# Kernel optimization log

Measured on AMD Instinct MI355X. Metric: run time of the kernel, lower is better.

The kernel has to match this reference:

```python
import jax, jax.numpy as jnp
import numpy as np

N_NODES = 100000
N_EDGES = 3200000
IN_DIM = 128
HID_DIM = 64
OUT_DIM = 2
N_GRAPHS = 512


def setup_inputs() -> dict:
    key = jax.random.key(0)
    ks = jax.random.split(key, 8)
    x = jax.random.normal(ks[0], (N_NODES, IN_DIM), dtype=jnp.float32)
    edge_index = jax.random.randint(ks[1], (2, N_EDGES), 0, N_NODES, dtype=jnp.int64)
    batch = jnp.sort(jax.random.randint(ks[2], (N_NODES,), 0, N_GRAPHS, dtype=jnp.int64))
    # GCNConv params (glorot-ish scale)
    W_gcn = jax.random.normal(ks[3], (IN_DIM, HID_DIM), dtype=jnp.float32) / np.sqrt(IN_DIM)
    b_gcn = jnp.zeros((HID_DIM,), dtype=jnp.float32)
    # MLP params: Linear(hid,hid) -> ReLU -> Linear(hid,out)
    W1 = jax.random.normal(ks[4], (HID_DIM, HID_DIM), dtype=jnp.float32) / np.sqrt(HID_DIM)
    b1 = jnp.zeros((HID_DIM,), dtype=jnp.float32)
    W2 = jax.random.normal(ks[5], (HID_DIM, OUT_DIM), dtype=jnp.float32) / np.sqrt(HID_DIM)
    b2 = jnp.zeros((OUT_DIM,), dtype=jnp.float32)
    return {"x": x, "edge_index": edge_index, "batch": batch,
            "W_gcn": W_gcn, "b_gcn": b_gcn, "W1": W1, "b1": b1, "W2": W2, "b2": b2}


def reference(x, edge_index, batch, W_gcn, b_gcn, W1, b1, W2, b2):
    n = x.shape[0]
    # --- GCNConv: add self-loops, symmetric normalization, aggregate, transform ---
    self_loop = jnp.arange(n, dtype=edge_index.dtype)
    row = jnp.concatenate([edge_index[0], self_loop])  # source nodes
    col = jnp.concatenate([edge_index[1], self_loop])  # target nodes
    deg = jax.ops.segment_sum(jnp.ones_like(col, dtype=x.dtype), col, num_segments=n)
    dinv = jnp.where(deg > 0, jax.lax.rsqrt(deg), 0.0)
    norm = dinv[row] * dinv[col]                       # (E+N,)
    xw = x @ W_gcn                                     # (N, hid) transform first (in_dim > hid)
    msg = xw[row] * norm[:, None]                      # gather + scale
    z = jax.ops.segment_sum(msg, col, num_segments=n) + b_gcn  # scatter-add
    z = jax.nn.relu(z)
    # --- global mean pool over graphs ---
    sums = jax.ops.segment_sum(z, batch, num_segments=N_GRAPHS)          # (G, hid)
    cnts = jax.ops.segment_sum(jnp.ones((n,), z.dtype), batch, num_segments=N_GRAPHS)
    g = sums / jnp.maximum(cnts, 1.0)[:, None]
    # --- MLP -> sigmoid ---
    h = jax.nn.relu(g @ W1 + b1)
    return jax.nn.sigmoid(h @ W2 + b2)                 # (G, out_dim)
```

## Files before the change

### kernel.cpp

```cpp
#include <hip/hip_runtime.h>

#define N_NODES 100000
#define N_EDGES 3200000
#define IN_DIM 128
#define HID_DIM 64
#define OUT_DIM 2
#define N_GRAPHS 512

#define BSHIFT 6
#define NBUCK 1564
#define NB3 256
#define EPB 12500
#define NSB 391
#define LDS_E2 3072
#define ZERO_ROW N_NODES

__device__ inline int xcol(int b) { return ((b & 7) << 5) | (b >> 3); }

__device__ inline float uaf(unsigned int u) {
    union { unsigned int i; float f; } v; v.i = u; return v.f;
}
__device__ inline unsigned short f2bf(float f) {
    union { float f; unsigned int i; } v; v.f = f;
    unsigned int r = v.i + 0x7fffu + ((v.i >> 16) & 1u);
    return (unsigned short)(r >> 16);
}

typedef __attribute__((ext_vector_type(8))) short bf16x8;
typedef __attribute__((ext_vector_type(4))) float f32x4;
typedef __attribute__((ext_vector_type(2))) float f32x2;

__global__ __launch_bounds__(512) void k_hist(const int* __restrict__ col,
                                              int* __restrict__ H) {
    __shared__ int h[NBUCK];
    for (int i = threadIdx.x; i < NBUCK; i += 512) h[i] = 0;
    __syncthreads();
    int b = blockIdx.x;
    int bb = xcol(b);
    int s = b * EPB, e = s + EPB;
    for (int i = s + threadIdx.x; i < e; i += 512)
        atomicAdd(&h[col[i] >> BSHIFT], 1);
    __syncthreads();
    for (int i = threadIdx.x; i < NBUCK; i += 512)
        H[i * NB3 + bb] = h[i];
}

__global__ __launch_bounds__(1024) void k_scan_a(const int* __restrict__ H,
                                                 int* __restrict__ OFF,
                                                 int* __restrict__ bsum) {
    __shared__ int lds[1024];
    int i = blockIdx.x * 1024 + threadIdx.x;
    int v = H[i];
    lds[threadIdx.x] = v;
    __syncthreads();
    for (int off = 1; off < 1024; off <<= 1) {
        int t = (threadIdx.x >= off) ? lds[threadIdx.x - off] : 0;
        __syncthreads();
        lds[threadIdx.x] += t;
        __syncthreads();
    }
    OFF[i] = lds[threadIdx.x] - v;
    if (threadIdx.x == 1023) bsum[blockIdx.x] = lds[1023];
}

__global__ __launch_bounds__(1024) void k_scan_b(int* __restrict__ OFF,
                                                 const int* __restrict__ bsum,
                                                 float* __restrict__ gsum,
                                                 unsigned char* __restrict__ xws) {
    __shared__ int ls[NSB];
    for (int i = threadIdx.x; i < NSB; i += 1024) ls[i] = bsum[i];
    __syncthreads();
    if (threadIdx.x == 0) {
        int run = 0;
        for (int b = 0; b < NSB; b++) { int t = ls[b]; ls[b] = run; run += t; }
    }
    __syncthreads();
    int i = blockIdx.x * 1024 + threadIdx.x;
    OFF[i] += ls[blockIdx.x];
    if (blockIdx.x < 32) gsum[blockIdx.x * 1024 + threadIdx.x] = 0.f;
    if (blockIdx.x == 32 && threadIdx.x < 16)
        ((int*)(xws + (size_t)ZERO_ROW * HID_DIM))[threadIdx.x] = 0;
}

__global__ __launch_bounds__(512) void k_scatter(const int* __restrict__ row,
                                                 const int* __restrict__ col,
                                                 const int* __restrict__ OFF,
                                                 int* __restrict__ binned) {
    __shared__ int lofs[NBUCK];
    __shared__ int cur[NBUCK];
    int b = blockIdx.x;
    int bb = xcol(b);
    for (int i = threadIdx.x; i < NBUCK; i += 512) {
        lofs[i] = OFF[i * NB3 + bb];
        cur[i] = 0;
    }
    __syncthreads();
    int s = b * EPB, e = s + EPB;
    for (int i = s + threadIdx.x; i < e; i += 512) {
        int c = col[i];
        int r = row[i];
        int bk = c >> BSHIFT;
        int rk = atomicAdd(&cur[bk], 1);
        binned[lofs[bk] + rk] = ((c & 63) << 17) | r;
    }
}

__global__ __launch_bounds__(256) void k_deg(const int* __restrict__ binned,
                                             const int* __restrict__ OFF,
                                             int* __restrict__ degs,
                                             float* __restrict__ dinv) {
    int bkt = blockIdx.x;
    int s = OFF[bkt * NB3];
    int e = (bkt == NBUCK - 1) ? N_EDGES : OFF[(bkt + 1) * NB3];
    __shared__ int cnt[64];
    if (threadIdx.x < 64) cnt[threadIdx.x] = 0;
    __syncthreads();
    for (int i = s + threadIdx.x; i < e; i += 256)
        atomicAdd(&cnt[binned[i] >> 17], 1);
    __syncthreads();
    int n = (bkt << BSHIFT) + threadIdx.x;
    if (threadIdx.x < 64 && n < N_NODES) {
        degs[n] = cnt[threadIdx.x];
        dinv[n] = rsqrtf((float)cnt[threadIdx.x] + 1.0f);
    }
}

__global__ __launch_bounds__(256) void k_gemm(const float* __restrict__ x,
                                              const float* __restrict__ Wg,
                                              const float* __restrict__ dinv,
                                              unsigned char* __restrict__ xws) {
    __shared__ unsigned short wb[16][64][8];

    for (int idx = threadIdx.x; idx < 1024; idx += 256) {
        int f = idx >> 6, l = idx & 63;
        int ks = f >> 2, nt = f & 3;
        int n = (l & 15) + (nt << 4);
        int kbase = (ks << 5) + ((l >> 4) << 3);
        unsigned short tmp[8];
#pragma unroll
        for (int j = 0; j < 8; j++)
            tmp[j] = f2bf(Wg[(kbase + j) * HID_DIM + n]);
        *(bf16x8*)&wb[f][l][0] = *(const bf16x8*)tmp;
    }
    __syncthreads();

    int wave = threadIdx.x >> 6;
    int lane = threadIdx.x & 63;
    int q = lane >> 4, nn = lane & 15;

    bf16x8 bfrag[4][4];
#pragma unroll
    for (int ks = 0; ks < 4; ks++)
#pragma unroll
        for (int nt = 0; nt < 4; nt++)
            bfrag[ks][nt] = *(const bf16x8*)&wb[ks * 4 + nt][lane][0];

    int node0 = blockIdx.x * 64 + wave * 16;
    int arow = node0 + nn;
    if (arow > N_NODES - 1) arow = N_NODES - 1;
    const float* xrow = x + (size_t)arow * IN_DIM + (q << 3);

    f32x4 acc[4] = {{0.f,0.f,0.f,0.f},{0.f,0.f,0.f,0.f},
                    {0.f,0.f,0.f,0.f},{0.f,0.f,0.f,0.f}};
#pragma unroll
    for (int ks = 0; ks < 4; ks++) {
        float4 xa = *(const float4*)(xrow + ks * 32);
        float4 xb_ = *(const float4*)(xrow + ks * 32 + 4);
        bf16x8 af;
        af[0] = (short)f2bf(xa.x); af[1] = (short)f2bf(xa.y);
        af[2] = (short)f2bf(xa.z); af[3] = (short)f2bf(xa.w);
        af[4] = (short)f2bf(xb_.x); af[5] = (short)f2bf(xb_.y);
        af[6] = (short)f2bf(xb_.z); af[7] = (short)f2bf(xb_.w);
#pragma unroll
        for (int nt = 0; nt < 4; nt++)
            acc[nt] = __builtin_amdgcn_mfma_f32_16x16x32_bf16(af, bfrag[ks][nt], acc[nt], 0, 0, 0);
    }

#pragma unroll
    for (int r = 0; r < 4; r++) {
        int mrow = node0 + q * 4 + r;
        if (mrow < N_NODES) {
            float dn = dinv[mrow];
            int p01 = __builtin_amdgcn_cvt_pk_fp8_f32(acc[0][r] * dn, acc[1][r] * dn, 0, false);
            int p23 = __builtin_amdgcn_cvt_pk_fp8_f32(acc[2][r] * dn, acc[3][r] * dn, 0, false);
            unsigned char* rp = xws + (size_t)mrow * HID_DIM + nn;
            rp[0]  = (unsigned char)(p01 & 0xff);
            rp[16] = (unsigned char)((p01 >> 8) & 0xff);
            rp[32] = (unsigned char)(p23 & 0xff);
            rp[48] = (unsigned char)((p23 >> 8) & 0xff);
        }
    }
}

__global__ __launch_bounds__(512) void k_aggrf(const unsigned char* __restrict__ xws,
                                               const int* __restrict__ binned,
                                               const int* __restrict__ OFF,
                                               const int* __restrict__ degs,
                                               const int* __restrict__ batch,
                                               const float* __restrict__ bg,
                                               float* __restrict__ gsum) {
    int bkt = blockIdx.x;
    int nbase = bkt << BSHIFT;
    if (nbase >= N_NODES) return;
    int nnodes = N_NODES - nbase; if (nnodes > 64) nnodes = 64;
    int s = OFF[bkt * NB3];
    int e = (bkt == NBUCK - 1) ? N_EDGES : OFF[(bkt + 1) * NB3];
    int m = e - s;

    __shared__ int cnt[64];
    __shared__ int lptr[65];
    __shared__ int cur[64];
    __shared__ int sb[64];
    __shared__ alignas(16) int srt[LDS_E2];
    __shared__ float pool[8][4][64];

    if (threadIdx.x < 64) {
        int n = nbase + threadIdx.x;
        cnt[threadIdx.x] = (threadIdx.x < nnodes) ? degs[n] : 0;
        sb[threadIdx.x]  = (threadIdx.x < nnodes) ? batch[n] : 0;
        cur[threadIdx.x] = 0;
    }
    for (int t = threadIdx.x; t < 8 * 4 * 64; t += 512)
        ((float*)pool)[t] = 0.f;
    __syncthreads();

    if (threadIdx.x == 0) {
        int run = 0;
        for (int i = 0; i < 64; i++) { lptr[i] = run; run += (cnt[i] + 15) & ~15; }
        lptr[64] = run;
    }
    __syncthreads();
    int tot = lptr[64]; if (tot > LDS_E2) tot = LDS_E2;
    for (int i = threadIdx.x; i < tot; i += 512) srt[i] = ZERO_ROW << 6;
    __syncthreads();
    for (int i = threadIdx.x; i < m; i += 512) {
        int pk = binned[s + i];
        int nid = pk >> 17;
        int rk = atomicAdd(&cur[nid], 1);
        int pos = lptr[nid] + rk;
        if (pos < LDS_E2) srt[pos] = (pk & 0x1FFFF) << 6;
    }
    __syncthreads();

    int wave = threadIdx.x >> 6;
    int lane = threadIdx.x & 63;
    int sub = lane >> 4;
    int lc  = lane & 15;
    int l4  = lc << 2;
    const unsigned char* xb = xws;
    float4 bg4 = ((const float4*)bg)[lc];
    int g0 = sb[0];

    for (int k = 0; k < 8; k++) {
        int ln = wave * 8 + k;
        if (ln >= nnodes) break;
        int n = nbase + ln;
        int s0 = lptr[ln], e0 = lptr[ln + 1];
        unsigned int ds = *(const unsigned int*)(xb + ((size_t)n << 6) + l4);
        f32x4 a0 = {0.f,0.f,0.f,0.f}, a1 = {0.f,0.f,0.f,0.f};
        f32x4 a2 = {0.f,0.f,0.f,0.f}, a3 = {0.f,0.f,0.f,0.f};
        for (int i = s0; i < e0; i += 16) {
            int4 r4 = *(const int4*)&srt[i + (sub << 2)];
            unsigned int d0 = *(const unsigned int*)(xb + r4.x + l4);
            unsigned int d1 = *(const unsigned int*)(xb + r4.y + l4);
            unsigned int d2 = *(const unsigned int*)(xb + r4.z + l4);
            unsigned int d3 = *(const unsigned int*)(xb + r4.w + l4);
            f32x2 p;
            p = __builtin_amdgcn_cvt_pk_f32_fp8(d0, false); a0[0] += p[0]; a0[1] += p[1];
            p = __builtin_amdgcn_cvt_pk_f32_fp8(d0, true);  a0[2] += p[0]; a0[3] += p[1];
            p = __builtin_amdgcn_cvt_pk_f32_fp8(d1, false); a1[0] += p[0]; a1[1] += p[1];
            p = __builtin_amdgcn_cvt_pk_f32_fp8(d1, true);  a1[2] += p[0]; a1[3] += p[1];
            p = __builtin_amdgcn_cvt_pk_f32_fp8(d2, false); a2[0] += p[0]; a2[1] += p[1];
            p = __builtin_amdgcn_cvt_pk_f32_fp8(d2, true);  a2[2] += p[0]; a2[3] += p[1];
            p = __builtin_amdgcn_cvt_pk_f32_fp8(d3, false); a3[0] += p[0]; a3[1] += p[1];
            p = __builtin_amdgcn_cvt_pk_f32_fp8(d3, true);  a3[2] += p[0]; a3[3] += p[1];
        }
        f32x4 t = (a0 + a1) + (a2 + a3);
#pragma unroll
        for (int c = 0; c < 4; c++) {
            float v = t[c];
            v += __shfl_xor(v, 16);
            v += __shfl_xor(v, 32);
            t[c] = v;
        }
        if (sub == 0) {
            f32x2 slo = __builtin_amdgcn_cvt_pk_f32_fp8(ds, false);
            f32x2 shi = __builtin_amdgcn_cvt_pk_f32_fp8(ds, true);
            t[0] += slo[0]; t[1] += slo[1]; t[2] += shi[0]; t[3] += shi[1];
            float dn = rsqrtf((float)cnt[ln] + 1.0f);
            float4 val;
            val.x = fmaxf(t[0] * dn + bg4.x, 0.f);
            val.y = fmaxf(t[1] * dn + bg4.y, 0.f);
            val.z = fmaxf(t[2] * dn + bg4.z, 0.f);
            val.w = fmaxf(t[3] * dn + bg4.w, 0.f);
            int slot = sb[ln] - g0;
            if (slot < 4) {
                float4* pp = (float4*)&pool[wave][slot][l4];
                float4 pv = *pp;
                pv.x += val.x; pv.y += val.y; pv.z += val.z; pv.w += val.w;
                *pp = pv;
            } else {
                atomicAdd(&gsum[sb[ln] * HID_DIM + l4 + 0], val.x);
                atomicAdd(&gsum[sb[ln] * HID_DIM + l4 + 1], val.y);
                atomicAdd(&gsum[sb[ln] * HID_DIM + l4 + 2], val.z);
                atomicAdd(&gsum[sb[ln] * HID_DIM + l4 + 3], val.w);
            }
        }
    }
    __syncthreads();

    for (int t = threadIdx.x; t < 4 * 64; t += 512) {
        int slot = t >> 6, j = t & 63;
        float v = 0.f;
#pragma unroll
        for (int w2 = 0; w2 < 8; w2++) v += pool[w2][slot][j];
        if (v != 0.f) atomicAdd(&gsum[(g0 + slot) * HID_DIM + j], v);
    }
}

__device__ inline int lower_bound_i(const int* __restrict__ a, int n, int v) {
    int lo = 0, hi = n;
    while (lo < hi) {
        int mid = (lo + hi) >> 1;
        if (a[mid] < v) lo = mid + 1; else hi = mid;
    }
    return lo;
}

__global__ __launch_bounds__(64) void k_mlp(const float* __restrict__ gsum,
                                            const int* __restrict__ batch,
                                            const float* __restrict__ W1,
                                            const float* __restrict__ b1,
                                            const float* __restrict__ W2,
                                            const float* __restrict__ b2,
                                            float* __restrict__ out) {
    int g = blockIdx.x;
    int j = threadIdx.x;
    int start = lower_bound_i(batch, N_NODES, g);
    int end   = lower_bound_i(batch, N_NODES, g + 1);
    float cnt = fmaxf((float)(end - start), 1.0f);

    __shared__ float gs[64];
    __shared__ float hs[64];
    gs[j] = gsum[g * 64 + j] / cnt;
    __syncthreads();

    float h = b1[j];
    for (int k = 0; k < 64; k++) h += gs[k] * W1[k * 64 + j];
    hs[j] = fmaxf(h, 0.f);
    __syncthreads();

    if (j < OUT_DIM) {
        float o = b2[j];
        for (int k = 0; k < 64; k++) o += hs[k] * W2[k * OUT_DIM + j];
        out[g * OUT_DIM + j] = 1.f / (1.f + expf(-o));
    }
}

extern "C" void kernel_launch(void* const* d_in, const int* in_sizes, int n_in,
                              void* d_out, int out_size, void* d_ws, size_t ws_size,
                              hipStream_t stream) {
    const float* x   = (const float*)d_in[0];
    const int* eidx  = (const int*)d_in[1];
    const int* batch = (const int*)d_in[2];
    const float* Wg  = (const float*)d_in[3];
    const float* bg  = (const float*)d_in[4];
    const float* W1  = (const float*)d_in[5];
    const float* b1  = (const float*)d_in[6];
    const float* W2  = (const float*)d_in[7];
    const float* b2  = (const float*)d_in[8];
    float* out = (float*)d_out;

    char* w = (char*)d_ws;
    unsigned char* xws = (unsigned char*)w;     w += (size_t)(N_NODES + 1) * HID_DIM;
    int*   binned  = (int*)w;                   w += (size_t)N_EDGES * 4;
    int*   H       = (int*)w;                   w += (size_t)NBUCK * NB3 * 4;
    int*   OFF     = (int*)w;                   w += (size_t)NBUCK * NB3 * 4;
    int*   bsum    = (int*)w;                   w += NSB * 4;
    int*   degs    = (int*)w;                   w += N_NODES * 4;
    float* dinv    = (float*)w;                 w += N_NODES * 4;
    float* gsum    = (float*)w;                 w += N_GRAPHS * HID_DIM * 4;

    const int* rowp = eidx;
    const int* colp = eidx + N_EDGES;

    k_hist<<<NB3, 512, 0, stream>>>(colp, H);
    k_scan_a<<<NSB, 1024, 0, stream>>>(H, OFF, bsum);
    k_scan_b<<<NSB, 1024, 0, stream>>>(OFF, bsum, gsum, xws);
    k_scatter<<<NB3, 512, 0, stream>>>(rowp, colp, OFF, binned);
    k_deg<<<NBUCK, 256, 0, stream>>>(binned, OFF, degs, dinv);
    k_gemm<<<(N_NODES + 63) / 64, 256, 0, stream>>>(x, Wg, dinv, xws);
    k_aggrf<<<NBUCK, 512, 0, stream>>>(xws, binned, OFF, degs, batch, bg, gsum);
    k_mlp<<<N_GRAPHS, 64, 0, stream>>>(gsum, batch, W1, b1, W2, b2, out);
}
```

Baseline: 213.3 us.

## Restructure aggregation kernel: 8-byte gathers, 256 threads, self-loop in LDS, fused graph counts

The aggregation kernel drops to 256 threads with 16 nodes per wave. Each lane now gathers 8 fp8 features as one uint2, two edges per sub-group, instead of four 4-byte loads. The self-loop is inserted as an extra entry in the LDS edge list, and the serial prefix sum over node slots is replaced by a wave shuffle scan. Per-graph node counts are accumulated in the aggregation kernel, so the MLP kernel no longer binary-searches the batch array. Fewer threads per block and fewer gathers in flight per wave may lower latency hiding in this gather-bound loop.

```diff
diff --git a/kernel.cpp b/kernel.cpp
--- a/kernel.cpp
+++ b/kernel.cpp
@@ -66,6 +66,7 @@
 __global__ __launch_bounds__(1024) void k_scan_b(int* __restrict__ OFF,
                                                  const int* __restrict__ bsum,
                                                  float* __restrict__ gsum,
+                                                 float* __restrict__ gcnt,
                                                  unsigned char* __restrict__ xws) {
     __shared__ int ls[NSB];
     for (int i = threadIdx.x; i < NSB; i += 1024) ls[i] = bsum[i];
@@ -78,6 +79,7 @@
     int i = blockIdx.x * 1024 + threadIdx.x;
     OFF[i] += ls[blockIdx.x];
     if (blockIdx.x < 32) gsum[blockIdx.x * 1024 + threadIdx.x] = 0.f;
+    if (blockIdx.x == 33 && threadIdx.x < N_GRAPHS) gcnt[threadIdx.x] = 0.f;
     if (blockIdx.x == 32 && threadIdx.x < 16)
         ((int*)(xws + (size_t)ZERO_ROW * HID_DIM))[threadIdx.x] = 0;
 }
@@ -192,13 +194,14 @@
     }
 }
 
-__global__ __launch_bounds__(512) void k_aggrf(const unsigned char* __restrict__ xws,
+__global__ __launch_bounds__(256) void k_aggrf(const unsigned char* __restrict__ xws,
                                                const int* __restrict__ binned,
                                                const int* __restrict__ OFF,
                                                const int* __restrict__ degs,
                                                const int* __restrict__ batch,
                                                const float* __restrict__ bg,
-                                               float* __restrict__ gsum) {
+                                               float* __restrict__ gsum,
+                                               float* __restrict__ gcnt) {
     int bkt = blockIdx.x;
     int nbase = bkt << BSHIFT;
     if (nbase >= N_NODES) return;
@@ -211,8 +214,9 @@
     __shared__ int lptr[65];
     __shared__ int cur[64];
     __shared__ int sb[64];
+    __shared__ float gcl[8];
     __shared__ alignas(16) int srt[LDS_E2];
-    __shared__ float pool[8][4][64];
+    __shared__ float pool[4][4][64];
 
     if (threadIdx.x < 64) {
         int n = nbase + threadIdx.x;
@@ -220,20 +224,34 @@
         sb[threadIdx.x]  = (threadIdx.x < nnodes) ? batch[n] : 0;
         cur[threadIdx.x] = 0;
     }
-    for (int t = threadIdx.x; t < 8 * 4 * 64; t += 512)
+    if (threadIdx.x < 8) gcl[threadIdx.x] = 0.f;
+    for (int t = threadIdx.x; t < 4 * 4 * 64; t += 256)
         ((float*)pool)[t] = 0.f;
     __syncthreads();
 
-    if (threadIdx.x == 0) {
-        int run = 0;
-        for (int i = 0; i < 64; i++) { lptr[i] = run; run += (cnt[i] + 15) & ~15; }
-        lptr[64] = run;
+    if (threadIdx.x < 64) {
+        int v = (cnt[threadIdx.x] + 16) & ~15;
+        int run = v;
+#pragma unroll
+        for (int off = 1; off < 64; off <<= 1) {
+            int t = __shfl_up(run, off);
+            if (threadIdx.x >= off) run += t;
+        }
+        lptr[threadIdx.x + 1] = run;
+        if (threadIdx.x == 0) lptr[0] = 0;
     }
     __syncthreads();
     int tot = lptr[64]; if (tot > LDS_E2) tot = LDS_E2;
-    for (int i = threadIdx.x; i < tot; i += 512) srt[i] = ZERO_ROW << 6;
-    __syncthreads();
-    for (int i = threadIdx.x; i < m; i += 512) {
+    for (int i = threadIdx.x; i < tot; i += 256) srt[i] = ZERO_ROW << 6;
+    __syncthreads();
+    if (threadIdx.x < nnodes) {
+        int p = lptr[threadIdx.x] + cnt[threadIdx.x];
+        if (p < LDS_E2) srt[p] = (nbase + threadIdx.x) << 6;
+        int sl = sb[threadIdx.x] - sb[0];
+        if (sl < 8) atomicAdd(&gcl[sl], 1.0f);
+        else atomicAdd(&gcnt[sb[threadIdx.x]], 1.0f);
+    }
+    for (int i = threadIdx.x; i < m; i += 256) {
         int pk = binned[s + i];
         int nid = pk >> 17;
         int rk = atomicAdd(&cur[nid], 1);
@@ -244,91 +262,84 @@
 
     int wave = threadIdx.x >> 6;
     int lane = threadIdx.x & 63;
-    int sub = lane >> 4;
-    int lc  = lane & 15;
-    int l4  = lc << 2;
-    const unsigned char* xb = xws;
-    float4 bg4 = ((const float4*)bg)[lc];
+    int sub = lane >> 3;
+    int lc  = lane & 7;
+    int l8  = lc << 3;
+    const unsigned char* xbl = xws + l8;
     int g0 = sb[0];
-
-    for (int k = 0; k < 8; k++) {
-        int ln = wave * 8 + k;
+    float4 bia0, bia1;
+    { const float4* bgv = (const float4*)bg;
+      bia0 = bgv[lc * 2]; bia1 = bgv[lc * 2 + 1]; }
+
+    for (int k = 0; k < 16; k++) {
+        int ln = wave * 16 + k;
         if (ln >= nnodes) break;
-        int n = nbase + ln;
         int s0 = lptr[ln], e0 = lptr[ln + 1];
-        unsigned int ds = *(const unsigned int*)(xb + ((size_t)n << 6) + l4);
-        f32x4 a0 = {0.f,0.f,0.f,0.f}, a1 = {0.f,0.f,0.f,0.f};
-        f32x4 a2 = {0.f,0.f,0.f,0.f}, a3 = {0.f,0.f,0.f,0.f};
+        if (s0 > LDS_E2) s0 = LDS_E2;
+        if (e0 > LDS_E2) e0 = LDS_E2;
+        f32x2 a0 = {0.f,0.f}, a1 = {0.f,0.f}, a2 = {0.f,0.f}, a3 = {0.f,0.f};
         for (int i = s0; i < e0; i += 16) {
-            int4 r4 = *(const int4*)&srt[i + (sub << 2)];
-            unsigned int d0 = *(const unsigned int*)(xb + r4.x + l4);
-            unsigned int d1 = *(const unsigned int*)(xb + r4.y + l4);
-            unsigned int d2 = *(const unsigned int*)(xb + r4.z + l4);
-            unsigned int d3 = *(const unsigned int*)(xb + r4.w + l4);
+            int2 rr = *(const int2*)&srt[i + (sub << 1)];
+            uint2 q0 = *(const uint2*)(xbl + rr.x);
+            uint2 q1 = *(const uint2*)(xbl + rr.y);
             f32x2 p;
-            p = __builtin_amdgcn_cvt_pk_f32_fp8(d0, false); a0[0] += p[0]; a0[1] += p[1];
-            p = __builtin_amdgcn_cvt_pk_f32_fp8(d0, true);  a0[2] += p[0]; a0[3] += p[1];
-            p = __builtin_amdgcn_cvt_pk_f32_fp8(d1, false); a1[0] += p[0]; a1[1] += p[1];
-            p = __builtin_amdgcn_cvt_pk_f32_fp8(d1, true);  a1[2] += p[0]; a1[3] += p[1];
-            p = __builtin_amdgcn_cvt_pk_f32_fp8(d2, false); a2[0] += p[0]; a2[1] += p[1];
-            p = __builtin_amdgcn_cvt_pk_f32_fp8(d2, true);  a2[2] += p[0]; a2[3] += p[1];
-            p = __builtin_amdgcn_cvt_pk_f32_fp8(d3, false); a3[0] += p[0]; a3[1] += p[1];
-            p = __builtin_amdgcn_cvt_pk_f32_fp8(d3, true);  a3[2] += p[0]; a3[3] += p[1];
+            p = __builtin_amdgcn_cvt_pk_f32_fp8(q0.x, false); a0 += p;
+            p = __builtin_amdgcn_cvt_pk_f32_fp8(q0.x, true);  a1 += p;
+            p = __builtin_amdgcn_cvt_pk_f32_fp8(q0.y, false); a2 += p;
+            p = __builtin_amdgcn_cvt_pk_f32_fp8(q0.y, true);  a3 += p;
+            p = __builtin_amdgcn_cvt_pk_f32_fp8(q1.x, false); a0 += p;
+            p = __builtin_amdgcn_cvt_pk_f32_fp8(q1.x, true);  a1 += p;
+            p = __builtin_amdgcn_cvt_pk_f32_fp8(q1.y, false); a2 += p;
+            p = __builtin_amdgcn_cvt_pk_f32_fp8(q1.y, true);  a3 += p;
         }
-        f32x4 t = (a0 + a1) + (a2 + a3);
-#pragma unroll
-        for (int c = 0; c < 4; c++) {
-            float v = t[c];
-            v += __shfl_xor(v, 16);
-            v += __shfl_xor(v, 32);
-            t[c] = v;
-        }
+        float r0 = a0[0], r1 = a0[1], r2 = a1[0], r3 = a1[1];
+        float r4 = a2[0], r5 = a2[1], r6 = a3[0], r7 = a3[1];
+#define RED8(x) x += __shfl_xor(x, 8); x += __shfl_xor(x, 16); x += __shfl_xor(x, 32);
+        RED8(r0) RED8(r1) RED8(r2) RED8(r3) RED8(r4) RED8(r5) RED8(r6) RED8(r7)
+#undef RED8
         if (sub == 0) {
-            f32x2 slo = __builtin_amdgcn_cvt_pk_f32_fp8(ds, false);
-            f32x2 shi = __builtin_amdgcn_cvt_pk_f32_fp8(ds, true);
-            t[0] += slo[0]; t[1] += slo[1]; t[2] += shi[0]; t[3] += shi[1];
             float dn = rsqrtf((float)cnt[ln] + 1.0f);
-            float4 val;
-            val.x = fmaxf(t[0] * dn + bg4.x, 0.f);
-            val.y = fmaxf(t[1] * dn + bg4.y, 0.f);
-            val.z = fmaxf(t[2] * dn + bg4.z, 0.f);
-            val.w = fmaxf(t[3] * dn + bg4.w, 0.f);
+            float4 v0, v1;
+            v0.x = fmaxf(r0 * dn + bia0.x, 0.f);
+            v0.y = fmaxf(r1 * dn + bia0.y, 0.f);
+            v0.z = fmaxf(r2 * dn + bia0.z, 0.f);
+            v0.w = fmaxf(r3 * dn + bia0.w, 0.f);
+            v1.x = fmaxf(r4 * dn + bia1.x, 0.f);
+            v1.y = fmaxf(r5 * dn + bia1.y, 0.f);
+            v1.z = fmaxf(r6 * dn + bia1.z, 0.f);
+            v1.w = fmaxf(r7 * dn + bia1.w, 0.f);
             int slot = sb[ln] - g0;
             if (slot < 4) {
-                float4* pp = (float4*)&pool[wave][slot][l4];
-                float4 pv = *pp;
-                pv.x += val.x; pv.y += val.y; pv.z += val.z; pv.w += val.w;
-                *pp = pv;
+                float4* pp = (float4*)&pool[wave][slot][l8];
+                float4 p0 = pp[0], p1 = pp[1];
+                p0.x += v0.x; p0.y += v0.y; p0.z += v0.z; p0.w += v0.w;
+                p1.x += v1.x; p1.y += v1.y; p1.z += v1.z; p1.w += v1.w;
+                pp[0] = p0; pp[1] = p1;
             } else {
-                atomicAdd(&gsum[sb[ln] * HID_DIM + l4 + 0], val.x);
-                atomicAdd(&gsum[sb[ln] * HID_DIM + l4 + 1], val.y);
-                atomicAdd(&gsum[sb[ln] * HID_DIM + l4 + 2], val.z);
-                atomicAdd(&gsum[sb[ln] * HID_DIM + l4 + 3], val.w);
+                float* gp = &gsum[sb[ln] * HID_DIM + l8];
+                atomicAdd(gp + 0, v0.x); atomicAdd(gp + 1, v0.y);
+                atomicAdd(gp + 2, v0.z); atomicAdd(gp + 3, v0.w);
+                atomicAdd(gp + 4, v1.x); atomicAdd(gp + 5, v1.y);
+                atomicAdd(gp + 6, v1.z); atomicAdd(gp + 7, v1.w);
             }
         }
     }
     __syncthreads();
 
-    for (int t = threadIdx.x; t < 4 * 64; t += 512) {
+    if (threadIdx.x < 8) {
+        float c = gcl[threadIdx.x];
+        if (c != 0.f) atomicAdd(&gcnt[g0 + threadIdx.x], c);
+    }
+    for (int t = threadIdx.x; t < 4 * 64; t += 256) {
         int slot = t >> 6, j = t & 63;
-        float v = 0.f;
-#pragma unroll
-        for (int w2 = 0; w2 < 8; w2++) v += pool[w2][slot][j];
+        float v = pool[0][slot][j] + pool[1][slot][j]
+                + pool[2][slot][j] + pool[3][slot][j];
         if (v != 0.f) atomicAdd(&gsum[(g0 + slot) * HID_DIM + j], v);
     }
 }
 
-__device__ inline int lower_bound_i(const int* __restrict__ a, int n, int v) {
-    int lo = 0, hi = n;
-    while (lo < hi) {
-        int mid = (lo + hi) >> 1;
-        if (a[mid] < v) lo = mid + 1; else hi = mid;
-    }
-    return lo;
-}
-
 __global__ __launch_bounds__(64) void k_mlp(const float* __restrict__ gsum,
-                                            const int* __restrict__ batch,
+                                            const float* __restrict__ gcnt,
                                             const float* __restrict__ W1,
                                             const float* __restrict__ b1,
                                             const float* __restrict__ W2,
@@ -336,9 +347,7 @@
                                             float* __restrict__ out) {
     int g = blockIdx.x;
     int j = threadIdx.x;
-    int start = lower_bound_i(batch, N_NODES, g);
-    int end   = lower_bound_i(batch, N_NODES, g + 1);
-    float cnt = fmaxf((float)(end - start), 1.0f);
+    float cnt = fmaxf(gcnt[g], 1.0f);
 
     __shared__ float gs[64];
     __shared__ float hs[64];
@@ -380,16 +389,17 @@
     int*   degs    = (int*)w;                   w += N_NODES * 4;
     float* dinv    = (float*)w;                 w += N_NODES * 4;
     float* gsum    = (float*)w;                 w += N_GRAPHS * HID_DIM * 4;
+    float* gcnt    = (float*)w;                 w += N_GRAPHS * 4;
 
     const int* rowp = eidx;
     const int* colp = eidx + N_EDGES;
 
     k_hist<<<NB3, 512, 0, stream>>>(colp, H);
     k_scan_a<<<NSB, 1024, 0, stream>>>(H, OFF, bsum);
-    k_scan_b<<<NSB, 1024, 0, stream>>>(OFF, bsum, gsum, xws);
+    k_scan_b<<<NSB, 1024, 0, stream>>>(OFF, bsum, gsum, gcnt, xws);
     k_scatter<<<NB3, 512, 0, stream>>>(rowp, colp, OFF, binned);
     k_deg<<<NBUCK, 256, 0, stream>>>(binned, OFF, degs, dinv);
     k_gemm<<<(N_NODES + 63) / 64, 256, 0, stream>>>(x, Wg, dinv, xws);
-    k_aggrf<<<NBUCK, 512, 0, stream>>>(xws, binned, OFF, degs, batch, bg, gsum);
-    k_mlp<<<N_GRAPHS, 64, 0, stream>>>(gsum, batch, W1, b1, W2, b2, out);
-}
+    k_aggrf<<<NBUCK, 256, 0, stream>>>(xws, binned, OFF, degs, batch, bg, gsum, gcnt);
+    k_mlp<<<N_GRAPHS, 64, 0, stream>>>(gsum, gcnt, W1, b1, W2, b2, out);
+}
```

Measured after the change: 221.4 us. 1.04x slower.
